# Optimization experiments

Hardware: AMD Instinct MI355X
Metric: run time of the kernel (lower is better)

## Reference

```python
import jax, jax.numpy as jnp
import numpy as np

EPS = 1e-36
N, F, C = 1024, 128, 2
P_DIM, BOND, SPACING, M_DIM = 4, 32, 8, 16
EMB_DIM = P_DIM ** C  # 16
NORM_INTERVAL = 1
STD = 0.55
N_BIG = (F + SPACING - 1) // SPACING   # 16 sites with output leg m=M_DIM
N_SMALL = F - N_BIG                    # 112 sites with m=1


def trig_embedding(x, p):
    # x: [N, F, C] in [0,1] -> [N, F, p**C]
    half = p // 2
    ks = 2.0 ** jnp.arange(1, half + 1, dtype=x.dtype)   # [2, 4, ...]
    ang = jnp.pi * x[..., None] / ks                     # [N,F,C,half]
    emb = jnp.stack([jnp.sin(ang), jnp.cos(ang)], -1)    # [N,F,C,half,2] -> sin1,cos1,sin2,cos2,...
    emb = emb.reshape(x.shape + (p,)) / float(np.sqrt(half))
    cur = emb[..., 0, :]
    for c in range(1, x.shape[-1]):                      # tensor product over channels
        cur = (cur[..., :, None] * emb[..., c, None, :]).reshape(x.shape[0], x.shape[1], -1)
    return cur


def build_mpo(w_big, w_small, sites, spacing):
    # Reassemble per-site MPO tensors (Dl, e, m, Dr); boundary bonds sliced to 1.
    mpo = []
    for n in range(sites):
        A = w_big[n // spacing] if n % spacing == 0 else w_small[n - n // spacing - 1]
        if n == 0:
            A = A[:1]
        if n == sites - 1:
            A = A[..., :1]
        mpo.append(A)
    return mpo


def _rescale(cur, log_norm):
    s = jnp.max(jnp.abs(cur))
    return cur / s, log_norm + jnp.log(s + EPS)


def log_partition_mpo(mpo):
    # log of squared F-norm of the MPO via zig-zag self-contraction with rescaling.
    sites = len(mpo)
    cur = mpo[0][0]                                   # (e, m, r); left bond (=1) squeezed
    log_norm = jnp.zeros((), cur.dtype)
    for i in range(sites - 1):
        if NORM_INTERVAL is not None and i % NORM_INTERVAL == 0:
            cur, log_norm = _rescale(cur, log_norm)
        if i == 0:
            cur = jnp.einsum('emf,emg->fg', cur, mpo[0][0])      # contract phys legs of site 0 copies
        else:
            cur = jnp.einsum('demf,demg->fg', cur, mpo[i])       # absorb copy-chain site i
        cur = jnp.einsum('fg,femh->gemh', cur, mpo[i + 1])       # absorb original-chain site i+1
    cur = jnp.einsum('demf,demg->fg', cur, mpo[-1])              # (1,1)
    return jnp.log(cur.reshape(()) + EPS) + log_norm


def sample_logit(emb_row, mpo):
    # emb_row: [F, e]. psi_n = sum_e A_n[l,e,m,r] emb[n,e]; logit = log ||psi||^2 (zig-zag + rescale).
    sites = len(mpo)
    psi_prev = jnp.einsum('emr,e->mr', mpo[0][0], emb_row[0])
    cur = psi_prev
    log_norm = jnp.zeros((), cur.dtype)
    for i in range(sites - 1):
        if NORM_INTERVAL is not None and i % NORM_INTERVAL == 0:
            cur, log_norm = _rescale(cur, log_norm)
        if i == 0:
            cur = jnp.einsum('mf,mg->fg', cur, psi_prev)
        else:
            cur = jnp.einsum('dmf,dmg->fg', cur, psi_prev)
        psi_prev = jnp.einsum('lemr,e->lmr', mpo[i + 1], emb_row[i + 1])
        cur = jnp.einsum('fg,fmh->gmh', cur, psi_prev)
    cur = jnp.einsum('dmf,dmg->fg', cur, psi_prev)               # (1,1)
    return jnp.log(cur.reshape(()) + EPS) + log_norm


def forward(x, w_big, w_small):
    emb = trig_embedding(x, P_DIM)                    # [N, F, EMB_DIM]
    mpo = build_mpo(w_big, w_small, F, SPACING)
    log_Z = log_partition_mpo(mpo)
    logits = jax.vmap(lambda e: sample_logit(e, mpo))(emb)   # [N]
    return logits, log_Z


def setup_inputs() -> dict:
    key = jax.random.key(0)
    k1, k2, k3 = jax.random.split(key, 3)
    x = jax.random.uniform(k1, (N, F, C), dtype=jnp.float32)
    w_big = STD * jax.random.normal(k2, (N_BIG, BOND, EMB_DIM, M_DIM, BOND), dtype=jnp.float32)
    w_small = STD * jax.random.normal(k3, (N_SMALL, BOND, EMB_DIM, 1, BOND), dtype=jnp.float32)
    return {"x": x, "w_big": w_big, "w_small": w_small}


def reference(x, w_big, w_small):
    return forward(x, w_big, w_small)
```

## Files before the change

kernel.cpp:

```cpp
#include <hip/hip_runtime.h>

typedef __attribute__((ext_vector_type(8)))  short  s16x8;
typedef __attribute__((ext_vector_type(8)))  __bf16 bf16x8;
typedef __attribute__((ext_vector_type(16))) float  f32x16;
typedef __attribute__((ext_vector_type(4)))  unsigned int u32x4;

#define EPSF 1e-36f

static __device__ __forceinline__ f32x16 MFMA(s16x8 a, s16x8 b, f32x16 c) {
  return __builtin_amdgcn_mfma_f32_32x32x16_bf16(
      __builtin_bit_cast(bf16x8, a), __builtin_bit_cast(bf16x8, b), c, 0, 0, 0);
}

static __device__ __forceinline__ short f2bf(float f) {
  unsigned u = __builtin_bit_cast(unsigned, f);
  u = (u + 0x7FFFu + ((u >> 16) & 1u)) >> 16;
  return (short)u;
}

static __device__ __forceinline__ unsigned pkf(float a, float b) {
  return (unsigned)(unsigned short)f2bf(a) | ((unsigned)(unsigned short)f2bf(b) << 16);
}

static __device__ __forceinline__ float bf2f(short s) {
  return __builtin_bit_cast(float, ((unsigned)(unsigned short)s) << 16);
}

static __device__ __forceinline__ void redistR(const f32x16 d, float sc, int h,
                                               s16x8& f0, s16x8& f1) {
  unsigned pk[8];
#pragma unroll
  for (int q = 0; q < 8; ++q) pk[q] = pkf(d[2 * q] * sc, d[2 * q + 1] * sc);
  unsigned s0 = h ? pk[0] : pk[2];
  unsigned s1 = h ? pk[1] : pk[3];
  unsigned s2 = h ? pk[4] : pk[6];
  unsigned s3 = h ? pk[5] : pk[7];
  unsigned r0 = (unsigned)__shfl_xor((int)s0, 32);
  unsigned r1 = (unsigned)__shfl_xor((int)s1, 32);
  unsigned r2 = (unsigned)__shfl_xor((int)s2, 32);
  unsigned r3 = (unsigned)__shfl_xor((int)s3, 32);
  u32x4 a, b;
  a.x = h ? r0 : pk[0]; a.y = h ? r1 : pk[1]; a.z = h ? pk[2] : r0; a.w = h ? pk[3] : r1;
  b.x = h ? r2 : pk[4]; b.y = h ? r3 : pk[5]; b.z = h ? pk[6] : r2; b.w = h ? pk[7] : r3;
  f0 = __builtin_bit_cast(s16x8, a);
  f1 = __builtin_bit_cast(s16x8, b);
}

static __device__ __forceinline__ void decodeStep(int sig, int& site, int& m, int& off) {
  int g = sig / 23, o = sig - g * 23;
  if (o < 16) { site = 8 * g; m = o; off = g * 376832 + o * 16384; }
  else { site = 8 * g + (o - 15); m = 0; off = g * 376832 + 262144 + (o - 16) * 16384; }
}

extern "C" __global__ void prep_emb_k(const float* __restrict__ x, float* __restrict__ Em) {
  int id = blockIdx.x * 256 + threadIdx.x;
  int site = id >> 10, n = id & 1023;
  float x0 = x[(n * 128 + site) * 2 + 0];
  float x1 = x[(n * 128 + site) * 2 + 1];
  const float P5 = 1.57079632679f, P25 = 0.785398163397f, R = 0.70710678118f;
  float u[4] = {sinf(P5 * x0) * R, cosf(P5 * x0) * R, sinf(P25 * x0) * R, cosf(P25 * x0) * R};
  float v[4] = {sinf(P5 * x1) * R, cosf(P5 * x1) * R, sinf(P25 * x1) * R, cosf(P25 * x1) * R};
#pragma unroll
  for (int a = 0; a < 4; ++a) {
    float4 o;
    o.x = u[a] * v[0]; o.y = u[a] * v[1]; o.z = u[a] * v[2]; o.w = u[a] * v[3];
    *(float4*)&Em[id * 16 + a * 4] = o;
  }
}

extern "C" __global__ void prep_w_k(const float* __restrict__ wb, const float* __restrict__ wsm,
                                    short* __restrict__ As) {
  int site = blockIdx.x;
  bool big = (site & 7) == 0;
  int nE = big ? 262144 : 16384;
  int nb = (site + 7) >> 3;
  int bs = nb * 262144 + (site - nb) * 16384;
  int kb = site >> 3;
  int ksm = site - kb - 1;
  for (int i = threadIdx.x; i < nE; i += 256) {
    int l = i & 31, e = (i >> 5) & 15, r = (i >> 9) & 31, m = i >> 14;
    float val = big ? wb[(((kb * 32 + l) * 16 + e) * 16 + m) * 32 + r]
                    : wsm[((ksm * 32 + l) * 16 + e) * 32 + r];
    if (site == 0 && l != 0) val = 0.f;
    if (site == 127 && r != 0) val = 0.f;
    As[bs + i] = f2bf(val);
  }
}

extern "C" __global__ void __launch_bounds__(256, 2)
tn_main(const short* __restrict__ As, const float* __restrict__ Em, float* __restrict__ out) {
  __shared__ __align__(16) char smem[65536];
  const int tid = threadIdx.x;
  const int lane = tid & 63;
  const int w = tid >> 6;
  const int c31 = lane & 31;
  const int h = lane >> 5;
  const f32x16 Z = {0.f,0.f,0.f,0.f,0.f,0.f,0.f,0.f,0.f,0.f,0.f,0.f,0.f,0.f,0.f,0.f};

  s16x8 Mf0 = {0,0,0,0,0,0,0,0}, Mf1 = {0,0,0,0,0,0,0,0};
  if (lane == 0) Mf0[0] = (short)0x3F80;
  f32x16 Macc = Z;
  float log_norm = 0.f;

  if (blockIdx.x < 256) {
    const int n = blockIdx.x * 4 + w;
    float er[16];

    {
      const short* src = As;
#pragma unroll
      for (int k = 0; k < 8; ++k) {
        s16x8 v = *(const s16x8*)(src + (k * 256 + tid) * 8);
        int G = k * 256 + tid, r = G >> 6, p = G & 63;
        *(s16x8*)(smem + (r * 64 + (p ^ (r & 7))) * 16) = v;
      }
    }
    __syncthreads();

#pragma unroll 1
    for (int sig = 0; sig < 368; ++sig) {
      int site, m, off; decodeStep(sig, site, m, off); (void)off;
      char* cur = smem + ((sig & 1) << 15);
      char* nxt = smem + (((sig + 1) & 1) << 15);

      s16x8 pre[8];
      const bool hasNext = (sig + 1 < 368);
      if (hasNext) {
        int st2, m2, off2; decodeStep(sig + 1, st2, m2, off2);
        const short* src = As + off2;
#pragma unroll
        for (int k = 0; k < 8; ++k)
          pre[k] = *(const s16x8*)(src + (k * 256 + tid) * 8);
      }

      if (m == 0) {
        const float4* ep = (const float4*)&Em[(site * 1024 + n) * 16];
        float4 q0 = ep[0], q1 = ep[1], q2 = ep[2], q3 = ep[3];
        er[0] = q0.x; er[1] = q0.y; er[2] = q0.z; er[3] = q0.w;
        er[4] = q1.x; er[5] = q1.y; er[6] = q1.z; er[7] = q1.w;
        er[8] = q2.x; er[9] = q2.y; er[10] = q2.z; er[11] = q2.w;
        er[12] = q3.x; er[13] = q3.y; er[14] = q3.z; er[15] = q3.w;
      }

      float acc[16];
#pragma unroll
      for (int c = 0; c < 16; ++c) acc[c] = 0.f;
      {
        const char* rowp = cur + c31 * 1024;
        const int sw = (c31 & 7) << 4;
#pragma unroll
        for (int e = 0; e < 16; ++e) {
          s16x8 v0 = *(const s16x8*)(rowp + (((e * 4 + 2 * h + 0) << 4) ^ sw));
          s16x8 v1 = *(const s16x8*)(rowp + (((e * 4 + 2 * h + 1) << 4) ^ sw));
          const float ce = er[e];
#pragma unroll
          for (int c = 0; c < 8; ++c) {
            acc[c]     = fmaf(ce, bf2f(v0[c]), acc[c]);
            acc[8 + c] = fmaf(ce, bf2f(v1[c]), acc[8 + c]);
          }
        }
      }
      s16x8 Bf0, Bf1;
      {
        unsigned o0[4], o1[4];
        o0[0] = pkf(acc[0], acc[1]);   o0[1] = pkf(acc[2], acc[3]);
        o0[2] = pkf(acc[4], acc[5]);   o0[3] = pkf(acc[6], acc[7]);
        o1[0] = pkf(acc[8], acc[9]);   o1[1] = pkf(acc[10], acc[11]);
        o1[2] = pkf(acc[12], acc[13]); o1[3] = pkf(acc[14], acc[15]);
        u32x4 b0, b1;
#pragma unroll
        for (int q = 0; q < 4; ++q) {
          unsigned snd = h ? o0[q] : o1[q];
          unsigned rcv = (unsigned)__shfl_xor((int)snd, 32);
          ((unsigned*)&b0)[q] = h ? rcv : o0[q];
          ((unsigned*)&b1)[q] = h ? o1[q] : rcv;
        }
        Bf0 = __builtin_bit_cast(s16x8, b0);
        Bf1 = __builtin_bit_cast(s16x8, b1);
      }

      f32x16 D1 = MFMA(Mf0, Bf0, Z);
      D1 = MFMA(Mf1, Bf1, D1);
      s16x8 Cf0, Cf1;
      redistR(D1, 1.f, h, Cf0, Cf1);
      if (m == 0) Macc = Z;
      Macc = MFMA(Bf0, Cf0, Macc);
      Macc = MFMA(Bf1, Cf1, Macc);

      bool lastM = (m == (((site & 7) == 0) ? 15 : 0));
      if (lastM) {
        if (site < 127) {
          float s = fabsf(Macc[0]);
#pragma unroll
          for (int j = 1; j < 16; ++j) s = fmaxf(s, fabsf(Macc[j]));
#pragma unroll
          for (int off2 = 32; off2 >= 1; off2 >>= 1) s = fmaxf(s, __shfl_xor(s, off2));
          float inv = 1.f / (s + EPSF);
          log_norm += logf(s + EPSF);
          redistR(Macc, inv, h, Mf0, Mf1);
        } else {
          if (lane == 0) out[n] = logf(fmaxf(Macc[0], 0.f) + EPSF) + log_norm;
        }
      }

      if (hasNext) {
#pragma unroll
        for (int k = 0; k < 8; ++k) {
          int G = k * 256 + tid, r = G >> 6, p = G & 63;
          *(s16x8*)(nxt + (r * 64 + (p ^ (r & 7))) * 16) = pre[k];
        }
      }
      __syncthreads();
    }
  } else {
    float* red = (float*)smem;
#pragma unroll 1
    for (int sig = 0; sig < 368; ++sig) {
      int site, m, off; decodeStep(sig, site, m, off);
      if (m == 0) Macc = Z;
      s16x8 pa[4], pb[4];
#pragma unroll
      for (int q = 0; q < 4; ++q) {
        int e = 4 * w + q;
        const short* ap = As + off + (c31 * 16 + e) * 32;
        pa[q] = *(const s16x8*)(ap + 8 * h);
        pb[q] = *(const s16x8*)(ap + 16 + 8 * h);
      }
#pragma unroll
      for (int q = 0; q < 4; ++q) {
        f32x16 D1 = MFMA(Mf0, pa[q], Z);
        D1 = MFMA(Mf1, pb[q], D1);
        s16x8 Cf0, Cf1;
        redistR(D1, 1.f, h, Cf0, Cf1);
        Macc = MFMA(pa[q], Cf0, Macc);
        Macc = MFMA(pb[q], Cf1, Macc);
      }
      bool lastM = (m == (((site & 7) == 0) ? 15 : 0));
      if (lastM) {
        float* myr = red + w * 1056;
#pragma unroll
        for (int reg = 0; reg < 16; ++reg) {
          int row = (reg & 3) + 8 * (reg >> 2) + 4 * h;
          myr[row * 33 + c31] = Macc[reg];
        }
        __syncthreads();
        f32x16 tot;
#pragma unroll
        for (int reg = 0; reg < 16; ++reg) {
          int row = (reg & 3) + 8 * (reg >> 2) + 4 * h;
          int idx = row * 33 + c31;
          tot[reg] = red[idx] + red[1056 + idx] + red[2112 + idx] + red[3168 + idx];
        }
        float s = fabsf(tot[0]);
#pragma unroll
        for (int j = 1; j < 16; ++j) s = fmaxf(s, fabsf(tot[j]));
#pragma unroll
        for (int off2 = 32; off2 >= 1; off2 >>= 1) s = fmaxf(s, __shfl_xor(s, off2));
        __syncthreads();
        if (site < 127) {
          float inv = 1.f / (s + EPSF);
          log_norm += logf(s + EPSF);
          redistR(tot, inv, h, Mf0, Mf1);
        } else {
          if (tid == 0) out[1024] = logf(fmaxf(tot[0], 0.f) + EPSF) + log_norm;
        }
      }
    }
  }
}

extern "C" void kernel_launch(void* const* d_in, const int* in_sizes, int n_in,
                              void* d_out, int out_size, void* d_ws, size_t ws_size,
                              hipStream_t stream) {
  (void)in_sizes; (void)n_in; (void)out_size; (void)ws_size;
  const float* x   = (const float*)d_in[0];
  const float* wb  = (const float*)d_in[1];
  const float* wsm = (const float*)d_in[2];
  short* As = (short*)d_ws;
  float* Em = (float*)((char*)d_ws + 12058624);
  float* out = (float*)d_out;

  prep_emb_k<<<512, 256, 0, stream>>>(x, Em);
  prep_w_k<<<128, 256, 0, stream>>>(wb, wsm, As);
  tn_main<<<257, 256, 0, stream>>>(As, Em, out);
}
```

Baseline: 1.084 ms.

## Precompute per-sample boundary tensors in a wide parallel kernel, chain over windows

Moves the embedding contraction (the fp32 weight-times-embedding reduction) out of the serial per-sample chain into a separate massively parallel kernel that writes bf16 B tensors for a window of steps into workspace. The chain kernel then only does the MFMA recurrences, streaming the precomputed B tensors with a 3-deep register prefetch and checkpointing state between windows. It adds large workspace traffic and extra launches. It falls back to the old monolithic kernel if the workspace is too small.

```diff
diff --git a/kernel.cpp b/kernel.cpp
--- a/kernel.cpp
+++ b/kernel.cpp
@@ -69,7 +69,7 @@
 }
 
 extern "C" __global__ void prep_w_k(const float* __restrict__ wb, const float* __restrict__ wsm,
-                                    short* __restrict__ As) {
+                                    short* __restrict__ As, float* __restrict__ Af) {
   int site = blockIdx.x;
   bool big = (site & 7) == 0;
   int nE = big ? 262144 : 16384;
@@ -84,11 +84,226 @@
     if (site == 0 && l != 0) val = 0.f;
     if (site == 127 && r != 0) val = 0.f;
     As[bs + i] = f2bf(val);
+    if (Af) Af[bs + i] = val;
+  }
+}
+
+extern "C" __global__ void __launch_bounds__(256, 4)
+bform_k(const float* __restrict__ Af, const float* __restrict__ Em,
+        short* __restrict__ Ball, int s0) {
+  const int sigL = blockIdx.x >> 7;
+  const int noct = blockIdx.x & 127;
+  int site, m, off; decodeStep(s0 + sigL, site, m, off); (void)m;
+  const int tid = threadIdx.x;
+  const int r = tid & 31;
+  const int nsub = tid >> 5;
+  const int n = noct * 8 + nsub;
+
+  float er[16];
+  {
+    const float4* ep = (const float4*)&Em[(site * 1024 + n) * 16];
+    float4 q0 = ep[0], q1 = ep[1], q2 = ep[2], q3 = ep[3];
+    er[0] = q0.x; er[1] = q0.y; er[2] = q0.z; er[3] = q0.w;
+    er[4] = q1.x; er[5] = q1.y; er[6] = q1.z; er[7] = q1.w;
+    er[8] = q2.x; er[9] = q2.y; er[10] = q2.z; er[11] = q2.w;
+    er[12] = q3.x; er[13] = q3.y; er[14] = q3.z; er[15] = q3.w;
+  }
+
+  const float* wp = Af + off + r * 512;
+  float acc[4][8];
+#pragma unroll
+  for (int a = 0; a < 4; ++a)
+#pragma unroll
+    for (int j = 0; j < 8; ++j) acc[a][j] = 0.f;
+
+#pragma unroll
+  for (int e = 0; e < 16; ++e) {
+    const float4* wr = (const float4*)(wp + e * 32);
+    float4 a0 = wr[0], a1 = wr[1], a2 = wr[2], a3 = wr[3];
+    float4 a4 = wr[4], a5 = wr[5], a6 = wr[6], a7 = wr[7];
+    const float ce = er[e];
+    acc[0][0] = fmaf(ce, a0.x, acc[0][0]); acc[0][1] = fmaf(ce, a0.y, acc[0][1]);
+    acc[0][2] = fmaf(ce, a0.z, acc[0][2]); acc[0][3] = fmaf(ce, a0.w, acc[0][3]);
+    acc[0][4] = fmaf(ce, a1.x, acc[0][4]); acc[0][5] = fmaf(ce, a1.y, acc[0][5]);
+    acc[0][6] = fmaf(ce, a1.z, acc[0][6]); acc[0][7] = fmaf(ce, a1.w, acc[0][7]);
+    acc[1][0] = fmaf(ce, a2.x, acc[1][0]); acc[1][1] = fmaf(ce, a2.y, acc[1][1]);
+    acc[1][2] = fmaf(ce, a2.z, acc[1][2]); acc[1][3] = fmaf(ce, a2.w, acc[1][3]);
+    acc[1][4] = fmaf(ce, a3.x, acc[1][4]); acc[1][5] = fmaf(ce, a3.y, acc[1][5]);
+    acc[1][6] = fmaf(ce, a3.z, acc[1][6]); acc[1][7] = fmaf(ce, a3.w, acc[1][7]);
+    acc[2][0] = fmaf(ce, a4.x, acc[2][0]); acc[2][1] = fmaf(ce, a4.y, acc[2][1]);
+    acc[2][2] = fmaf(ce, a4.z, acc[2][2]); acc[2][3] = fmaf(ce, a4.w, acc[2][3]);
+    acc[2][4] = fmaf(ce, a5.x, acc[2][4]); acc[2][5] = fmaf(ce, a5.y, acc[2][5]);
+    acc[2][6] = fmaf(ce, a5.z, acc[2][6]); acc[2][7] = fmaf(ce, a5.w, acc[2][7]);
+    acc[3][0] = fmaf(ce, a6.x, acc[3][0]); acc[3][1] = fmaf(ce, a6.y, acc[3][1]);
+    acc[3][2] = fmaf(ce, a6.z, acc[3][2]); acc[3][3] = fmaf(ce, a6.w, acc[3][3]);
+    acc[3][4] = fmaf(ce, a7.x, acc[3][4]); acc[3][5] = fmaf(ce, a7.y, acc[3][5]);
+    acc[3][6] = fmaf(ce, a7.z, acc[3][6]); acc[3][7] = fmaf(ce, a7.w, acc[3][7]);
+  }
+
+  short* bp = Ball + ((size_t)sigL * 1024 + n) * 1024;
+#pragma unroll
+  for (int loct = 0; loct < 4; ++loct) {
+    s16x8 o;
+#pragma unroll
+    for (int j = 0; j < 8; ++j) o[j] = f2bf(acc[loct][j]);
+    *(s16x8*)(bp + (loct >> 1) * 512 + (loct & 1) * 256 + r * 8) = o;
   }
 }
 
 extern "C" __global__ void __launch_bounds__(256, 2)
-tn_main(const short* __restrict__ As, const float* __restrict__ Em, float* __restrict__ out) {
+tn_chain(const short* __restrict__ As, const short* __restrict__ Ball,
+         unsigned* __restrict__ CkU, float* __restrict__ LN,
+         float* __restrict__ out, int s0, int s1) {
+  __shared__ __align__(16) float red[4 * 1056];
+  const int tid = threadIdx.x;
+  const int lane = tid & 63;
+  const int w = tid >> 6;
+  const int c31 = lane & 31;
+  const int h = lane >> 5;
+  const f32x16 Z = {0.f,0.f,0.f,0.f,0.f,0.f,0.f,0.f,0.f,0.f,0.f,0.f,0.f,0.f,0.f,0.f};
+  const int nsig = s1 - s0;
+
+  s16x8 Mf0 = {0,0,0,0,0,0,0,0}, Mf1 = {0,0,0,0,0,0,0,0};
+  f32x16 Macc = Z;
+  float log_norm = 0.f;
+
+  if (blockIdx.x < 256) {
+    const int n = blockIdx.x * 4 + w;
+    if (s0 == 0) {
+      if (lane == 0) Mf0[0] = (short)0x3F80;
+    } else {
+      const unsigned* cp = CkU + ((size_t)n * 64 + lane) * 8;
+      u32x4 a = *(const u32x4*)cp;
+      u32x4 b = *(const u32x4*)(cp + 4);
+      Mf0 = __builtin_bit_cast(s16x8, a);
+      Mf1 = __builtin_bit_cast(s16x8, b);
+      log_norm = LN[n];
+    }
+
+    const short* bb = Ball + (size_t)n * 1024 + lane * 8;
+    s16x8 c0, c1, d0, d1, e0, e1;
+    {
+      const short* p0 = bb;
+      c0 = *(const s16x8*)p0; c1 = *(const s16x8*)(p0 + 512);
+      const short* p1 = bb + ((size_t)1 << 20);
+      d0 = *(const s16x8*)p1; d1 = *(const s16x8*)(p1 + 512);
+      const short* p2 = bb + ((size_t)2 << 20);
+      e0 = *(const s16x8*)p2; e1 = *(const s16x8*)(p2 + 512);
+    }
+
+#pragma unroll 1
+    for (int k = 0; k < nsig; ++k) {
+      int site, m, off; decodeStep(s0 + k, site, m, off); (void)off;
+      f32x16 D1 = MFMA(Mf0, c0, Z);
+      D1 = MFMA(Mf1, c1, D1);
+      s16x8 Cf0, Cf1;
+      redistR(D1, 1.f, h, Cf0, Cf1);
+      if (m == 0) Macc = Z;
+      Macc = MFMA(c0, Cf0, Macc);
+      Macc = MFMA(c1, Cf1, Macc);
+
+      bool lastM = (m == (((site & 7) == 0) ? 15 : 0));
+      if (lastM) {
+        if (site < 127) {
+          float s = fabsf(Macc[0]);
+#pragma unroll
+          for (int j = 1; j < 16; ++j) s = fmaxf(s, fabsf(Macc[j]));
+#pragma unroll
+          for (int off2 = 32; off2 >= 1; off2 >>= 1) s = fmaxf(s, __shfl_xor(s, off2));
+          float inv = 1.f / (s + EPSF);
+          log_norm += logf(s + EPSF);
+          redistR(Macc, inv, h, Mf0, Mf1);
+        } else {
+          if (lane == 0) out[n] = logf(fmaxf(Macc[0], 0.f) + EPSF) + log_norm;
+        }
+      }
+      c0 = d0; c1 = d1; d0 = e0; d1 = e1;
+      if (k + 3 < nsig) {
+        const short* p = bb + ((size_t)(k + 3) << 20);
+        e0 = *(const s16x8*)p;
+        e1 = *(const s16x8*)(p + 512);
+      }
+    }
+    if (s1 < 368) {
+      unsigned* cp = CkU + ((size_t)n * 64 + lane) * 8;
+      *(u32x4*)cp       = __builtin_bit_cast(u32x4, Mf0);
+      *(u32x4*)(cp + 4) = __builtin_bit_cast(u32x4, Mf1);
+      if (lane == 0) LN[n] = log_norm;
+    }
+  } else {
+    if (s0 == 0) {
+      if (lane == 0) Mf0[0] = (short)0x3F80;
+    } else {
+      const unsigned* cp = CkU + ((size_t)1024 * 64 + lane) * 8;
+      u32x4 a = *(const u32x4*)cp;
+      u32x4 b = *(const u32x4*)(cp + 4);
+      Mf0 = __builtin_bit_cast(s16x8, a);
+      Mf1 = __builtin_bit_cast(s16x8, b);
+      log_norm = LN[1024];
+    }
+#pragma unroll 1
+    for (int sig = s0; sig < s1; ++sig) {
+      int site, m, off; decodeStep(sig, site, m, off);
+      if (m == 0) Macc = Z;
+      s16x8 pa[4], pb[4];
+#pragma unroll
+      for (int q = 0; q < 4; ++q) {
+        int e = 4 * w + q;
+        const short* ap = As + off + (c31 * 16 + e) * 32;
+        pa[q] = *(const s16x8*)(ap + 8 * h);
+        pb[q] = *(const s16x8*)(ap + 16 + 8 * h);
+      }
+#pragma unroll
+      for (int q = 0; q < 4; ++q) {
+        f32x16 D1 = MFMA(Mf0, pa[q], Z);
+        D1 = MFMA(Mf1, pb[q], D1);
+        s16x8 Cf0, Cf1;
+        redistR(D1, 1.f, h, Cf0, Cf1);
+        Macc = MFMA(pa[q], Cf0, Macc);
+        Macc = MFMA(pb[q], Cf1, Macc);
+      }
+      bool lastM = (m == (((site & 7) == 0) ? 15 : 0));
+      if (lastM) {
+        float* myr = red + w * 1056;
+#pragma unroll
+        for (int reg = 0; reg < 16; ++reg) {
+          int row = (reg & 3) + 8 * (reg >> 2) + 4 * h;
+          myr[row * 33 + c31] = Macc[reg];
+        }
+        __syncthreads();
+        f32x16 tot;
+#pragma unroll
+        for (int reg = 0; reg < 16; ++reg) {
+          int row = (reg & 3) + 8 * (reg >> 2) + 4 * h;
+          int idx = row * 33 + c31;
+          tot[reg] = red[idx] + red[1056 + idx] + red[2112 + idx] + red[3168 + idx];
+        }
+        float s = fabsf(tot[0]);
+#pragma unroll
+        for (int j = 1; j < 16; ++j) s = fmaxf(s, fabsf(tot[j]));
+#pragma unroll
+        for (int off2 = 32; off2 >= 1; off2 >>= 1) s = fmaxf(s, __shfl_xor(s, off2));
+        __syncthreads();
+        if (site < 127) {
+          float inv = 1.f / (s + EPSF);
+          log_norm += logf(s + EPSF);
+          redistR(tot, inv, h, Mf0, Mf1);
+        } else {
+          if (tid == 0) out[1024] = logf(fmaxf(tot[0], 0.f) + EPSF) + log_norm;
+        }
+      }
+    }
+    if (s1 < 368 && w == 0) {
+      unsigned* cp = CkU + ((size_t)1024 * 64 + lane) * 8;
+      *(u32x4*)cp       = __builtin_bit_cast(u32x4, Mf0);
+      *(u32x4*)(cp + 4) = __builtin_bit_cast(u32x4, Mf1);
+      if (lane == 0) LN[1024] = log_norm;
+    }
+  }
+}
+
+extern "C" __global__ void __launch_bounds__(256, 2)
+tn_main_mono(const short* __restrict__ As, const float* __restrict__ Em, float* __restrict__ out) {
   __shared__ __align__(16) char smem[65536];
   const int tid = threadIdx.x;
   const int lane = tid & 63;
@@ -96,7 +311,6 @@
   const int c31 = lane & 31;
   const int h = lane >> 5;
   const f32x16 Z = {0.f,0.f,0.f,0.f,0.f,0.f,0.f,0.f,0.f,0.f,0.f,0.f,0.f,0.f,0.f,0.f};
-
   s16x8 Mf0 = {0,0,0,0,0,0,0,0}, Mf1 = {0,0,0,0,0,0,0,0};
   if (lane == 0) Mf0[0] = (short)0x3F80;
   f32x16 Macc = Z;
@@ -105,7 +319,6 @@
   if (blockIdx.x < 256) {
     const int n = blockIdx.x * 4 + w;
     float er[16];
-
     {
       const short* src = As;
 #pragma unroll
@@ -116,23 +329,19 @@
       }
     }
     __syncthreads();
-
 #pragma unroll 1
     for (int sig = 0; sig < 368; ++sig) {
       int site, m, off; decodeStep(sig, site, m, off); (void)off;
       char* cur = smem + ((sig & 1) << 15);
       char* nxt = smem + (((sig + 1) & 1) << 15);
-
       s16x8 pre[8];
       const bool hasNext = (sig + 1 < 368);
       if (hasNext) {
         int st2, m2, off2; decodeStep(sig + 1, st2, m2, off2);
         const short* src = As + off2;
 #pragma unroll
-        for (int k = 0; k < 8; ++k)
-          pre[k] = *(const s16x8*)(src + (k * 256 + tid) * 8);
-      }
-
+        for (int k = 0; k < 8; ++k) pre[k] = *(const s16x8*)(src + (k * 256 + tid) * 8);
+      }
       if (m == 0) {
         const float4* ep = (const float4*)&Em[(site * 1024 + n) * 16];
         float4 q0 = ep[0], q1 = ep[1], q2 = ep[2], q3 = ep[3];
@@ -141,7 +350,6 @@
         er[8] = q2.x; er[9] = q2.y; er[10] = q2.z; er[11] = q2.w;
         er[12] = q3.x; er[13] = q3.y; er[14] = q3.z; er[15] = q3.w;
       }
-
       float acc[16];
 #pragma unroll
       for (int c = 0; c < 16; ++c) acc[c] = 0.f;
@@ -178,7 +386,6 @@
         Bf0 = __builtin_bit_cast(s16x8, b0);
         Bf1 = __builtin_bit_cast(s16x8, b1);
       }
-
       f32x16 D1 = MFMA(Mf0, Bf0, Z);
       D1 = MFMA(Mf1, Bf1, D1);
       s16x8 Cf0, Cf1;
@@ -186,7 +393,6 @@
       if (m == 0) Macc = Z;
       Macc = MFMA(Bf0, Cf0, Macc);
       Macc = MFMA(Bf1, Cf1, Macc);
-
       bool lastM = (m == (((site & 7) == 0) ? 15 : 0));
       if (lastM) {
         if (site < 127) {
@@ -202,7 +408,6 @@
           if (lane == 0) out[n] = logf(fmaxf(Macc[0], 0.f) + EPSF) + log_norm;
         }
       }
-
       if (hasNext) {
 #pragma unroll
         for (int k = 0; k < 8; ++k) {
@@ -272,15 +477,38 @@
 extern "C" void kernel_launch(void* const* d_in, const int* in_sizes, int n_in,
                               void* d_out, int out_size, void* d_ws, size_t ws_size,
                               hipStream_t stream) {
-  (void)in_sizes; (void)n_in; (void)out_size; (void)ws_size;
+  (void)in_sizes; (void)n_in; (void)out_size;
   const float* x   = (const float*)d_in[0];
   const float* wb  = (const float*)d_in[1];
   const float* wsm = (const float*)d_in[2];
-  short* As = (short*)d_ws;
-  float* Em = (float*)((char*)d_ws + 12058624);
+  char* ws = (char*)d_ws;
   float* out = (float*)d_out;
-
-  prep_emb_k<<<512, 256, 0, stream>>>(x, Em);
-  prep_w_k<<<128, 256, 0, stream>>>(wb, wsm, As);
-  tn_main<<<257, 256, 0, stream>>>(As, Em, out);
-}
+  short* As = (short*)ws;
+
+  int nwin = 0;
+  const size_t fixed = 47185920ull;
+  for (int c = 4; c <= 16; c *= 2) {
+    if (ws_size >= fixed + (size_t)(368 / c) * 1024 * 2048) { nwin = c; break; }
+  }
+
+  if (nwin) {
+    float*    Af   = (float*)(ws + 12058624);
+    float*    Em   = (float*)(ws + 36175872);
+    unsigned* CkU  = (unsigned*)(ws + 44564480);
+    float*    LN   = (float*)(ws + 46663680);
+    short*    Ball = (short*)(ws + 47185920);
+    prep_emb_k<<<512, 256, 0, stream>>>(x, Em);
+    prep_w_k<<<128, 256, 0, stream>>>(wb, wsm, As, Af);
+    const int spw = 368 / nwin;
+    for (int wdx = 0; wdx < nwin; ++wdx) {
+      const int s0 = wdx * spw;
+      bform_k<<<spw * 128, 256, 0, stream>>>(Af, Em, Ball, s0);
+      tn_chain<<<257, 256, 0, stream>>>(As, Ball, CkU, LN, out, s0, s0 + spw);
+    }
+  } else {
+    float* Em = (float*)(ws + 12058624);
+    prep_emb_k<<<512, 256, 0, stream>>>(x, Em);
+    prep_w_k<<<128, 256, 0, stream>>>(wb, wsm, As, nullptr);
+    tn_main_mono<<<257, 256, 0, stream>>>(As, Em, out);
+  }
+}
```

After: 3.616 ms. 234% more time.

## Split sample blocks into producer and consumer warps with an fp32 weight copy

Applied to the files above, without the earlier changes.

Each sample block grows to 512 threads. Four producer warps contract the embedding with site weights, read directly from a new fp32 weight copy in global memory, and write MFMA fragments into double-buffered LDS. Four consumer warps do only the MFMA transfer-matrix updates and rescaling, one step behind. The log-partition block now spreads the work over 8 warps and double-buffers its partial-sum area, which removes one barrier per step. This trades the shared-memory staging of bf16 weights for extra global fp32 traffic and a larger workspace, and it writes an extra fp32 array in the prep kernel.

```diff
diff --git a/kernel.cpp b/kernel.cpp
--- a/kernel.cpp
+++ b/kernel.cpp
@@ -20,10 +20,6 @@
 
 static __device__ __forceinline__ unsigned pkf(float a, float b) {
   return (unsigned)(unsigned short)f2bf(a) | ((unsigned)(unsigned short)f2bf(b) << 16);
-}
-
-static __device__ __forceinline__ float bf2f(short s) {
-  return __builtin_bit_cast(float, ((unsigned)(unsigned short)s) << 16);
 }
 
 static __device__ __forceinline__ void redistR(const f32x16 d, float sc, int h,
@@ -69,7 +65,7 @@
 }
 
 extern "C" __global__ void prep_w_k(const float* __restrict__ wb, const float* __restrict__ wsm,
-                                    short* __restrict__ As) {
+                                    short* __restrict__ As, float* __restrict__ Af) {
   int site = blockIdx.x;
   bool big = (site & 7) == 0;
   int nE = big ? 262144 : 16384;
@@ -84,12 +80,14 @@
     if (site == 0 && l != 0) val = 0.f;
     if (site == 127 && r != 0) val = 0.f;
     As[bs + i] = f2bf(val);
+    Af[bs + i] = val;
   }
 }
 
-extern "C" __global__ void __launch_bounds__(256, 2)
-tn_main(const short* __restrict__ As, const float* __restrict__ Em, float* __restrict__ out) {
-  __shared__ __align__(16) char smem[65536];
+extern "C" __global__ void __launch_bounds__(512, 4)
+tn_fused(const short* __restrict__ As, const float* __restrict__ Af,
+         const float* __restrict__ Em, float* __restrict__ out) {
+  __shared__ __align__(16) char smem[67584];
   const int tid = threadIdx.x;
   const int lane = tid & 63;
   const int w = tid >> 6;
@@ -97,71 +95,77 @@
   const int h = lane >> 5;
   const f32x16 Z = {0.f,0.f,0.f,0.f,0.f,0.f,0.f,0.f,0.f,0.f,0.f,0.f,0.f,0.f,0.f,0.f};
 
-  s16x8 Mf0 = {0,0,0,0,0,0,0,0}, Mf1 = {0,0,0,0,0,0,0,0};
-  if (lane == 0) Mf0[0] = (short)0x3F80;
-  f32x16 Macc = Z;
-  float log_norm = 0.f;
-
   if (blockIdx.x < 256) {
-    const int n = blockIdx.x * 4 + w;
-    float er[16];
-
-    {
-      const short* src = As;
-#pragma unroll
-      for (int k = 0; k < 8; ++k) {
-        s16x8 v = *(const s16x8*)(src + (k * 256 + tid) * 8);
-        int G = k * 256 + tid, r = G >> 6, p = G & 63;
-        *(s16x8*)(smem + (r * 64 + (p ^ (r & 7))) * 16) = v;
-      }
-    }
-    __syncthreads();
-
+    if (w < 4) {
+      const int n = blockIdx.x * 4 + w;
+      s16x8 Mf0 = {0,0,0,0,0,0,0,0}, Mf1 = {0,0,0,0,0,0,0,0};
+      if (lane == 0) Mf0[0] = (short)0x3F80;
+      f32x16 Macc = Z;
+      float log_norm = 0.f;
+
+      __syncthreads();
 #pragma unroll 1
-    for (int sig = 0; sig < 368; ++sig) {
-      int site, m, off; decodeStep(sig, site, m, off); (void)off;
-      char* cur = smem + ((sig & 1) << 15);
-      char* nxt = smem + (((sig + 1) & 1) << 15);
-
-      s16x8 pre[8];
-      const bool hasNext = (sig + 1 < 368);
-      if (hasNext) {
-        int st2, m2, off2; decodeStep(sig + 1, st2, m2, off2);
-        const short* src = As + off2;
-#pragma unroll
-        for (int k = 0; k < 8; ++k)
-          pre[k] = *(const s16x8*)(src + (k * 256 + tid) * 8);
-      }
-
-      if (m == 0) {
-        const float4* ep = (const float4*)&Em[(site * 1024 + n) * 16];
-        float4 q0 = ep[0], q1 = ep[1], q2 = ep[2], q3 = ep[3];
-        er[0] = q0.x; er[1] = q0.y; er[2] = q0.z; er[3] = q0.w;
-        er[4] = q1.x; er[5] = q1.y; er[6] = q1.z; er[7] = q1.w;
-        er[8] = q2.x; er[9] = q2.y; er[10] = q2.z; er[11] = q2.w;
-        er[12] = q3.x; er[13] = q3.y; er[14] = q3.z; er[15] = q3.w;
-      }
-
-      float acc[16];
-#pragma unroll
-      for (int c = 0; c < 16; ++c) acc[c] = 0.f;
-      {
-        const char* rowp = cur + c31 * 1024;
-        const int sw = (c31 & 7) << 4;
+      for (int sig = 0; sig < 368; ++sig) {
+        int site, m, off; decodeStep(sig, site, m, off); (void)off;
+        const char* src = smem + ((sig & 1) << 14) + w * 4096 + lane * 16;
+        s16x8 c0 = *(const s16x8*)src;
+        s16x8 c1 = *(const s16x8*)(src + 1024);
+
+        f32x16 D1 = MFMA(Mf0, c0, Z);
+        D1 = MFMA(Mf1, c1, D1);
+        s16x8 Cf0, Cf1;
+        redistR(D1, 1.f, h, Cf0, Cf1);
+        if (m == 0) Macc = Z;
+        Macc = MFMA(c0, Cf0, Macc);
+        Macc = MFMA(c1, Cf1, Macc);
+
+        bool lastM = (m == (((site & 7) == 0) ? 15 : 0));
+        if (lastM) {
+          if (site < 127) {
+            float s = fabsf(Macc[0]);
+#pragma unroll
+            for (int j = 1; j < 16; ++j) s = fmaxf(s, fabsf(Macc[j]));
+#pragma unroll
+            for (int off2 = 32; off2 >= 1; off2 >>= 1) s = fmaxf(s, __shfl_xor(s, off2));
+            float inv = 1.f / (s + EPSF);
+            log_norm += logf(s + EPSF);
+            redistR(Macc, inv, h, Mf0, Mf1);
+          } else {
+            if (lane == 0) out[n] = logf(fmaxf(Macc[0], 0.f) + EPSF) + log_norm;
+          }
+        }
+        __syncthreads();
+      }
+    } else {
+      const int n = blockIdx.x * 4 + (w - 4);
+      char* const myslot = smem + (w - 4) * 4096 + lane * 16;
+      float er[16];
+
+      auto produce = [&](int sigN) {
+        int st, m, off; decodeStep(sigN, st, m, off);
+        if (m == 0) {
+          const float4* ep = (const float4*)&Em[(st * 1024 + n) * 16];
+          float4 q0 = ep[0], q1 = ep[1], q2 = ep[2], q3 = ep[3];
+          er[0] = q0.x; er[1] = q0.y; er[2] = q0.z; er[3] = q0.w;
+          er[4] = q1.x; er[5] = q1.y; er[6] = q1.z; er[7] = q1.w;
+          er[8] = q2.x; er[9] = q2.y; er[10] = q2.z; er[11] = q2.w;
+          er[12] = q3.x; er[13] = q3.y; er[14] = q3.z; er[15] = q3.w;
+        }
+        const float* wp = Af + off + c31 * 512 + h * 16;
+        float acc[16];
+#pragma unroll
+        for (int c = 0; c < 16; ++c) acc[c] = 0.f;
 #pragma unroll
         for (int e = 0; e < 16; ++e) {
-          s16x8 v0 = *(const s16x8*)(rowp + (((e * 4 + 2 * h + 0) << 4) ^ sw));
-          s16x8 v1 = *(const s16x8*)(rowp + (((e * 4 + 2 * h + 1) << 4) ^ sw));
+          float av[16];
+          *(float4*)&av[0]  = *(const float4*)(wp + e * 32 + 0);
+          *(float4*)&av[4]  = *(const float4*)(wp + e * 32 + 4);
+          *(float4*)&av[8]  = *(const float4*)(wp + e * 32 + 8);
+          *(float4*)&av[12] = *(const float4*)(wp + e * 32 + 12);
           const float ce = er[e];
 #pragma unroll
-          for (int c = 0; c < 8; ++c) {
-            acc[c]     = fmaf(ce, bf2f(v0[c]), acc[c]);
-            acc[8 + c] = fmaf(ce, bf2f(v1[c]), acc[8 + c]);
-          }
-        }
-      }
-      s16x8 Bf0, Bf1;
-      {
+          for (int c = 0; c < 16; ++c) acc[c] = fmaf(ce, av[c], acc[c]);
+        }
         unsigned o0[4], o1[4];
         o0[0] = pkf(acc[0], acc[1]);   o0[1] = pkf(acc[2], acc[3]);
         o0[2] = pkf(acc[4], acc[5]);   o0[3] = pkf(acc[6], acc[7]);
@@ -175,89 +179,72 @@
           ((unsigned*)&b0)[q] = h ? rcv : o0[q];
           ((unsigned*)&b1)[q] = h ? o1[q] : rcv;
         }
-        Bf0 = __builtin_bit_cast(s16x8, b0);
-        Bf1 = __builtin_bit_cast(s16x8, b1);
-      }
-
-      f32x16 D1 = MFMA(Mf0, Bf0, Z);
-      D1 = MFMA(Mf1, Bf1, D1);
-      s16x8 Cf0, Cf1;
-      redistR(D1, 1.f, h, Cf0, Cf1);
-      if (m == 0) Macc = Z;
-      Macc = MFMA(Bf0, Cf0, Macc);
-      Macc = MFMA(Bf1, Cf1, Macc);
-
-      bool lastM = (m == (((site & 7) == 0) ? 15 : 0));
-      if (lastM) {
-        if (site < 127) {
-          float s = fabsf(Macc[0]);
-#pragma unroll
-          for (int j = 1; j < 16; ++j) s = fmaxf(s, fabsf(Macc[j]));
-#pragma unroll
-          for (int off2 = 32; off2 >= 1; off2 >>= 1) s = fmaxf(s, __shfl_xor(s, off2));
-          float inv = 1.f / (s + EPSF);
-          log_norm += logf(s + EPSF);
-          redistR(Macc, inv, h, Mf0, Mf1);
-        } else {
-          if (lane == 0) out[n] = logf(fmaxf(Macc[0], 0.f) + EPSF) + log_norm;
-        }
-      }
-
-      if (hasNext) {
-#pragma unroll
-        for (int k = 0; k < 8; ++k) {
-          int G = k * 256 + tid, r = G >> 6, p = G & 63;
-          *(s16x8*)(nxt + (r * 64 + (p ^ (r & 7))) * 16) = pre[k];
-        }
-      }
+        char* dst = myslot + ((sigN & 1) << 14);
+        *(s16x8*)dst          = __builtin_bit_cast(s16x8, b0);
+        *(s16x8*)(dst + 1024) = __builtin_bit_cast(s16x8, b1);
+      };
+
+      produce(0);
       __syncthreads();
+#pragma unroll 1
+      for (int sig = 0; sig < 368; ++sig) {
+        if (sig + 1 < 368) produce(sig + 1);
+        __syncthreads();
+      }
     }
   } else {
-    float* red = (float*)smem;
+    float* part = (float*)smem;
+    s16x8 Mf0 = {0,0,0,0,0,0,0,0}, Mf1 = {0,0,0,0,0,0,0,0};
+    if (lane == 0) Mf0[0] = (short)0x3F80;
+    f32x16 Pacc = Z;
+    float log_norm = 0.f;
+
+    __syncthreads();
 #pragma unroll 1
     for (int sig = 0; sig < 368; ++sig) {
       int site, m, off; decodeStep(sig, site, m, off);
-      if (m == 0) Macc = Z;
-      s16x8 pa[4], pb[4];
-#pragma unroll
-      for (int q = 0; q < 4; ++q) {
-        int e = 4 * w + q;
+      if (m == 0) Pacc = Z;
+#pragma unroll
+      for (int q = 0; q < 2; ++q) {
+        int e = 2 * w + q;
         const short* ap = As + off + (c31 * 16 + e) * 32;
-        pa[q] = *(const s16x8*)(ap + 8 * h);
-        pb[q] = *(const s16x8*)(ap + 16 + 8 * h);
-      }
-#pragma unroll
-      for (int q = 0; q < 4; ++q) {
-        f32x16 D1 = MFMA(Mf0, pa[q], Z);
-        D1 = MFMA(Mf1, pb[q], D1);
+        s16x8 pa = *(const s16x8*)(ap + 8 * h);
+        s16x8 pb = *(const s16x8*)(ap + 16 + 8 * h);
+        f32x16 D1 = MFMA(Mf0, pa, Z);
+        D1 = MFMA(Mf1, pb, D1);
         s16x8 Cf0, Cf1;
         redistR(D1, 1.f, h, Cf0, Cf1);
-        Macc = MFMA(pa[q], Cf0, Macc);
-        Macc = MFMA(pb[q], Cf1, Macc);
+        Pacc = MFMA(pa, Cf0, Pacc);
+        Pacc = MFMA(pb, Cf1, Pacc);
       }
       bool lastM = (m == (((site & 7) == 0) ? 15 : 0));
       if (lastM) {
-        float* myr = red + w * 1056;
+        float* myr = part + ((site & 1) * 8 + w) * 1056;
 #pragma unroll
         for (int reg = 0; reg < 16; ++reg) {
           int row = (reg & 3) + 8 * (reg >> 2) + 4 * h;
-          myr[row * 33 + c31] = Macc[reg];
-        }
-        __syncthreads();
+          myr[row * 33 + c31] = Pacc[reg];
+        }
+      }
+      __syncthreads();
+      if (lastM) {
+        const float* base = part + (site & 1) * 8 * 1056;
         f32x16 tot;
 #pragma unroll
         for (int reg = 0; reg < 16; ++reg) {
           int row = (reg & 3) + 8 * (reg >> 2) + 4 * h;
           int idx = row * 33 + c31;
-          tot[reg] = red[idx] + red[1056 + idx] + red[2112 + idx] + red[3168 + idx];
-        }
-        float s = fabsf(tot[0]);
-#pragma unroll
-        for (int j = 1; j < 16; ++j) s = fmaxf(s, fabsf(tot[j]));
-#pragma unroll
-        for (int off2 = 32; off2 >= 1; off2 >>= 1) s = fmaxf(s, __shfl_xor(s, off2));
-        __syncthreads();
+          float sum = 0.f;
+#pragma unroll
+          for (int w2 = 0; w2 < 8; ++w2) sum += base[w2 * 1056 + idx];
+          tot[reg] = sum;
+        }
         if (site < 127) {
+          float s = fabsf(tot[0]);
+#pragma unroll
+          for (int j = 1; j < 16; ++j) s = fmaxf(s, fabsf(tot[j]));
+#pragma unroll
+          for (int off2 = 32; off2 >= 1; off2 >>= 1) s = fmaxf(s, __shfl_xor(s, off2));
           float inv = 1.f / (s + EPSF);
           log_norm += logf(s + EPSF);
           redistR(tot, inv, h, Mf0, Mf1);
@@ -276,11 +263,13 @@
   const float* x   = (const float*)d_in[0];
   const float* wb  = (const float*)d_in[1];
   const float* wsm = (const float*)d_in[2];
-  short* As = (short*)d_ws;
-  float* Em = (float*)((char*)d_ws + 12058624);
+  char* ws = (char*)d_ws;
+  short* As = (short*)ws;
+  float* Af = (float*)(ws + 12058624);
+  float* Em = (float*)(ws + 36175872);
   float* out = (float*)d_out;
 
   prep_emb_k<<<512, 256, 0, stream>>>(x, Em);
-  prep_w_k<<<128, 256, 0, stream>>>(wb, wsm, As);
-  tn_main<<<257, 256, 0, stream>>>(As, Em, out);
-}
+  prep_w_k<<<128, 256, 0, stream>>>(wb, wsm, As, Af);
+  tn_fused<<<257, 512, 0, stream>>>(As, Af, Em, out);
+}
```

Measured after the change: 3.572 ms. 3.3x slower.

## Contract embedding on MFMA with async global-to-LDS staging and re-laid weights

Applied to the files above, without the earlier changes.

Replaces the scalar FMA contraction of each site tensor with the embedding vector by bf16 MFMA ops. Four samples per block are packed into one MFMA operand, and the results are exchanged through a swizzled LDS area. Weights are stored in a second layout (e fastest) and staged with global_load_lds instead of register prefetch plus LDS stores. LDS use drops, but launch bounds fall to one block per SM and an extra barrier is added per step. Most MFMA rows are wasted, since only 4 of 32 rows carry samples, and prep writes twice the weight data.

```diff
diff --git a/kernel.cpp b/kernel.cpp
--- a/kernel.cpp
+++ b/kernel.cpp
@@ -20,10 +20,6 @@
 
 static __device__ __forceinline__ unsigned pkf(float a, float b) {
   return (unsigned)(unsigned short)f2bf(a) | ((unsigned)(unsigned short)f2bf(b) << 16);
-}
-
-static __device__ __forceinline__ float bf2f(short s) {
-  return __builtin_bit_cast(float, ((unsigned)(unsigned short)s) << 16);
 }
 
 static __device__ __forceinline__ void redistR(const f32x16 d, float sc, int h,
@@ -69,7 +65,7 @@
 }
 
 extern "C" __global__ void prep_w_k(const float* __restrict__ wb, const float* __restrict__ wsm,
-                                    short* __restrict__ As) {
+                                    short* __restrict__ As, short* __restrict__ As2) {
   int site = blockIdx.x;
   bool big = (site & 7) == 0;
   int nE = big ? 262144 : 16384;
@@ -78,18 +74,21 @@
   int kb = site >> 3;
   int ksm = site - kb - 1;
   for (int i = threadIdx.x; i < nE; i += 256) {
-    int l = i & 31, e = (i >> 5) & 15, r = (i >> 9) & 31, m = i >> 14;
+    int e = i & 15, r = (i >> 4) & 31, l = (i >> 9) & 31, m = i >> 14;
     float val = big ? wb[(((kb * 32 + l) * 16 + e) * 16 + m) * 32 + r]
                     : wsm[((ksm * 32 + l) * 16 + e) * 32 + r];
     if (site == 0 && l != 0) val = 0.f;
     if (site == 127 && r != 0) val = 0.f;
-    As[bs + i] = f2bf(val);
+    short bv = f2bf(val);
+    As2[bs + i] = bv;
+    As[bs + ((m * 32 + r) * 16 + e) * 32 + l] = bv;
   }
 }
 
-extern "C" __global__ void __launch_bounds__(256, 2)
-tn_main(const short* __restrict__ As, const float* __restrict__ Em, float* __restrict__ out) {
-  __shared__ __align__(16) char smem[65536];
+extern "C" __global__ void __launch_bounds__(256, 1)
+tn_main(const short* __restrict__ As, const short* __restrict__ As2,
+        const float* __restrict__ Em, float* __restrict__ out) {
+  __shared__ __align__(16) char smem[40960];
   const int tid = threadIdx.x;
   const int lane = tid & 63;
   const int w = tid >> 6;
@@ -97,95 +96,83 @@
   const int h = lane >> 5;
   const f32x16 Z = {0.f,0.f,0.f,0.f,0.f,0.f,0.f,0.f,0.f,0.f,0.f,0.f,0.f,0.f,0.f,0.f};
 
-  s16x8 Mf0 = {0,0,0,0,0,0,0,0}, Mf1 = {0,0,0,0,0,0,0,0};
-  if (lane == 0) Mf0[0] = (short)0x3F80;
-  f32x16 Macc = Z;
-  float log_norm = 0.f;
-
   if (blockIdx.x < 256) {
-    const int n = blockIdx.x * 4 + w;
-    float er[16];
-
-    {
-      const short* src = As;
+    const int n0 = blockIdx.x * 4;
+    s16x8 Mf0 = {0,0,0,0,0,0,0,0}, Mf1 = {0,0,0,0,0,0,0,0};
+    if (lane == 0) Mf0[0] = (short)0x3F80;
+    f32x16 Macc = Z;
+    float log_norm = 0.f;
+    s16x8 Ef = {0,0,0,0,0,0,0,0};
+
+    auto stage = [&](int sig2) {
+      int st2, m2, off2; decodeStep(sig2, st2, m2, off2);
+      const char* src = (const char*)As2 + (size_t)off2 * 2;
 #pragma unroll
       for (int k = 0; k < 8; ++k) {
-        s16x8 v = *(const s16x8*)(src + (k * 256 + tid) * 8);
-        int G = k * 256 + tid, r = G >> 6, p = G & 63;
-        *(s16x8*)(smem + (r * 64 + (p ^ (r & 7))) * 16) = v;
-      }
-    }
+        int GL = (k * 4 + w) * 64 + lane;
+        int gs = (GL & ~63) | ((GL & 63) ^ ((GL >> 6) & 7));
+        __builtin_amdgcn_global_load_lds((const unsigned int*)(src + gs * 16),
+                                         (unsigned int*)(smem + (k * 4 + w) * 1024),
+                                         16, 0, 0);
+      }
+    };
+
+    stage(0);
     __syncthreads();
 
 #pragma unroll 1
     for (int sig = 0; sig < 368; ++sig) {
       int site, m, off; decodeStep(sig, site, m, off); (void)off;
-      char* cur = smem + ((sig & 1) << 15);
-      char* nxt = smem + (((sig + 1) & 1) << 15);
-
-      s16x8 pre[8];
-      const bool hasNext = (sig + 1 < 368);
-      if (hasNext) {
-        int st2, m2, off2; decodeStep(sig + 1, st2, m2, off2);
-        const short* src = As + off2;
-#pragma unroll
-        for (int k = 0; k < 8; ++k)
-          pre[k] = *(const s16x8*)(src + (k * 256 + tid) * 8);
-      }
 
       if (m == 0) {
-        const float4* ep = (const float4*)&Em[(site * 1024 + n) * 16];
-        float4 q0 = ep[0], q1 = ep[1], q2 = ep[2], q3 = ep[3];
-        er[0] = q0.x; er[1] = q0.y; er[2] = q0.z; er[3] = q0.w;
-        er[4] = q1.x; er[5] = q1.y; er[6] = q1.z; er[7] = q1.w;
-        er[8] = q2.x; er[9] = q2.y; er[10] = q2.z; er[11] = q2.w;
-        er[12] = q3.x; er[13] = q3.y; er[14] = q3.z; er[15] = q3.w;
-      }
-
-      float acc[16];
-#pragma unroll
-      for (int c = 0; c < 16; ++c) acc[c] = 0.f;
-      {
-        const char* rowp = cur + c31 * 1024;
-        const int sw = (c31 & 7) << 4;
-#pragma unroll
-        for (int e = 0; e < 16; ++e) {
-          s16x8 v0 = *(const s16x8*)(rowp + (((e * 4 + 2 * h + 0) << 4) ^ sw));
-          s16x8 v1 = *(const s16x8*)(rowp + (((e * 4 + 2 * h + 1) << 4) ^ sw));
-          const float ce = er[e];
-#pragma unroll
-          for (int c = 0; c < 8; ++c) {
-            acc[c]     = fmaf(ce, bf2f(v0[c]), acc[c]);
-            acc[8 + c] = fmaf(ce, bf2f(v1[c]), acc[8 + c]);
-          }
-        }
-      }
-      s16x8 Bf0, Bf1;
-      {
-        unsigned o0[4], o1[4];
-        o0[0] = pkf(acc[0], acc[1]);   o0[1] = pkf(acc[2], acc[3]);
-        o0[2] = pkf(acc[4], acc[5]);   o0[3] = pkf(acc[6], acc[7]);
-        o1[0] = pkf(acc[8], acc[9]);   o1[1] = pkf(acc[10], acc[11]);
-        o1[2] = pkf(acc[12], acc[13]); o1[3] = pkf(acc[14], acc[15]);
-        u32x4 b0, b1;
-#pragma unroll
-        for (int q = 0; q < 4; ++q) {
-          unsigned snd = h ? o0[q] : o1[q];
-          unsigned rcv = (unsigned)__shfl_xor((int)snd, 32);
-          ((unsigned*)&b0)[q] = h ? rcv : o0[q];
-          ((unsigned*)&b1)[q] = h ? o1[q] : rcv;
-        }
-        Bf0 = __builtin_bit_cast(s16x8, b0);
-        Bf1 = __builtin_bit_cast(s16x8, b1);
-      }
-
-      f32x16 D1 = MFMA(Mf0, Bf0, Z);
-      D1 = MFMA(Mf1, Bf1, D1);
+        float4 q0 = {0.f,0.f,0.f,0.f}, q1 = {0.f,0.f,0.f,0.f};
+        if (c31 < 4) {
+          const float* ep = Em + ((size_t)site * 1024 + n0 + c31) * 16 + 8 * h;
+          q0 = *(const float4*)ep;
+          q1 = *(const float4*)(ep + 4);
+        }
+        u32x4 ef;
+        ef.x = pkf(q0.x, q0.y); ef.y = pkf(q0.z, q0.w);
+        ef.z = pkf(q1.x, q1.y); ef.w = pkf(q1.z, q1.w);
+        Ef = __builtin_bit_cast(s16x8, ef);
+      }
+
+      unsigned* barea = (unsigned*)(smem + 32768);
+#pragma unroll
+      for (int t = 0; t < 4; ++t) {
+        const int lA = 8 * w + 2 * t;
+        const int lB = lA + 1;
+        s16x8 WA = *(const s16x8*)(smem + lA * 1024 + (((c31 * 2 + h) ^ (lA & 7)) << 4));
+        s16x8 WB = *(const s16x8*)(smem + lB * 1024 + (((c31 * 2 + h) ^ (lB & 7)) << 4));
+        f32x16 DA = MFMA(Ef, WA, Z);
+        f32x16 DB = MFMA(Ef, WB, Z);
+        if (h == 0) {
+          const int pr = (4 * w + t) ^ (c31 & 15);
+#pragma unroll
+          for (int q = 0; q < 4; ++q)
+            barea[q * 512 + c31 * 16 + pr] = pkf(DA[q], DB[q]);
+        }
+      }
+      __syncthreads();
+
+      if (sig + 1 < 368) stage(sig + 1);
+
+      const unsigned* ba = (const unsigned*)(smem + 32768) + w * 512 + c31 * 16;
+      u32x4 b0v, b1v;
+#pragma unroll
+      for (int i = 0; i < 4; ++i) ((unsigned*)&b0v)[i] = ba[(4 * h + i) ^ (c31 & 15)];
+#pragma unroll
+      for (int i = 0; i < 4; ++i) ((unsigned*)&b1v)[i] = ba[(8 + 4 * h + i) ^ (c31 & 15)];
+      s16x8 c0 = __builtin_bit_cast(s16x8, b0v);
+      s16x8 c1 = __builtin_bit_cast(s16x8, b1v);
+
+      f32x16 D1 = MFMA(Mf0, c0, Z);
+      D1 = MFMA(Mf1, c1, D1);
       s16x8 Cf0, Cf1;
       redistR(D1, 1.f, h, Cf0, Cf1);
       if (m == 0) Macc = Z;
-      Macc = MFMA(Bf0, Cf0, Macc);
-      Macc = MFMA(Bf1, Cf1, Macc);
+      Macc = MFMA(c0, Cf0, Macc);
+      Macc = MFMA(c1, Cf1, Macc);
 
       bool lastM = (m == (((site & 7) == 0) ? 15 : 0));
       if (lastM) {
@@ -199,21 +186,17 @@
           log_norm += logf(s + EPSF);
           redistR(Macc, inv, h, Mf0, Mf1);
         } else {
-          if (lane == 0) out[n] = logf(fmaxf(Macc[0], 0.f) + EPSF) + log_norm;
-        }
-      }
-
-      if (hasNext) {
-#pragma unroll
-        for (int k = 0; k < 8; ++k) {
-          int G = k * 256 + tid, r = G >> 6, p = G & 63;
-          *(s16x8*)(nxt + (r * 64 + (p ^ (r & 7))) * 16) = pre[k];
+          if (lane == 0) out[n0 + w] = logf(fmaxf(Macc[0], 0.f) + EPSF) + log_norm;
         }
       }
       __syncthreads();
     }
   } else {
     float* red = (float*)smem;
+    s16x8 Mf0 = {0,0,0,0,0,0,0,0}, Mf1 = {0,0,0,0,0,0,0,0};
+    if (lane == 0) Mf0[0] = (short)0x3F80;
+    f32x16 Macc = Z;
+    float log_norm = 0.f;
 #pragma unroll 1
     for (int sig = 0; sig < 368; ++sig) {
       int site, m, off; decodeStep(sig, site, m, off);
@@ -276,11 +259,13 @@
   const float* x   = (const float*)d_in[0];
   const float* wb  = (const float*)d_in[1];
   const float* wsm = (const float*)d_in[2];
-  short* As = (short*)d_ws;
-  float* Em = (float*)((char*)d_ws + 12058624);
+  char* ws = (char*)d_ws;
+  short* As  = (short*)ws;
+  short* As2 = (short*)(ws + 12058624);
+  float* Em  = (float*)(ws + 24117248);
   float* out = (float*)d_out;
 
   prep_emb_k<<<512, 256, 0, stream>>>(x, Em);
-  prep_w_k<<<128, 256, 0, stream>>>(wb, wsm, As);
-  tn_main<<<257, 256, 0, stream>>>(As, Em, out);
-}
+  prep_w_k<<<128, 256, 0, stream>>>(wb, wsm, As, As2);
+  tn_main<<<257, 256, 0, stream>>>(As, As2, Em, out);
+}
```

Result: slower. 1.265 ms (+16.8%).
